# Performance work log

Measured on AMD Instinct MI355X. Metric: run time of the kernel, lower is better.

The kernel has to match this reference:

```python
import jax, jax.numpy as jnp
import numpy as np

BIG = 10000000.0

def heaviside(x):
    return (jnp.tanh(BIG * x) + 1.0) * 0.5

def interception(Prec, PET, INSC):
    INSC = jnp.clip(INSC * 5.0, 0.5, 5.0)
    IMAX = jnp.maximum(jnp.minimum(INSC, PET), 0.0)
    INT = jnp.maximum(jnp.minimum(IMAX, Prec), 0.0)
    INR = jnp.maximum(Prec - INT, 0.0)
    return INT, INR

def soil_moisture_store(SMS1, SMSC):
    SMSC = jnp.clip(SMSC * 500.0, 50.0, 500.0)
    return jnp.maximum(jnp.minimum(SMS1, SMSC), 0.0)

def soil_fluxes(PET, INT, INR, COEFF, SQ, SMSC, SUB, CRAK, SMS1):
    COEFF = jnp.clip(COEFF * 400.0, 50.0, 400.0)
    SQ = jnp.clip(SQ * 6.0, 0.0, 6.0)
    SMSC = jnp.clip(SMSC * 500.0, 50.0, 500.0)
    SUB = jnp.clip(SUB, 0.0, 1.0)
    CRAK = jnp.clip(CRAK, 0.0, 1.0)
    cap = COEFF * jnp.exp(-SQ * SMS1 / SMSC)
    RMO = jnp.maximum(heaviside(cap - INR) * INR + heaviside(INR - cap) * cap, 0.0)
    IRUN = jnp.maximum(INR - RMO, 0.0)
    SRUN = jnp.maximum(SUB * (SMS1 / SMSC) * RMO, 0.0)
    REC = jnp.maximum(CRAK * (SMS1 / SMSC) * (RMO - SRUN), 0.0)
    SMF = jnp.maximum(RMO - SRUN - REC, 0.0)
    POT = jnp.maximum(PET - INT, 0.0)
    r = 10.0 * SMS1 / SMSC
    ETS = jnp.maximum(heaviside(r - POT) * POT + heaviside(POT - r) * r, 0.0)
    return RMO, IRUN, SRUN, REC, SMF, ETS

def recharge_calculation(SMS1, SMSC, REC, SMF, ETS):
    SMSC = jnp.clip(SMSC * 500.0, 50.0, 500.0)
    s = SMS1 + SMF - ETS
    RECnew = heaviside(s - SMSC) * (REC + s - SMSC) + heaviside(SMSC - s) * REC
    return jnp.maximum(RECnew, 0.0)

def groundwaterstore(GW1, RecK):
    RecK = jnp.clip(RecK * 0.3, 0.003, 0.3)
    return jnp.maximum(heaviside(GW1) * (RecK * GW1), 0.0)

def _forward(inputs, INSC, COEFF, SQ, SMSC, SUB, CRAK, RecK):
    B, T, _ = inputs.shape
    xs = jnp.transpose(inputs, (1, 0, 2))  # (T, B, 2)

    def step(carry, x):
        SMS1, GW1 = carry  # each (B, 1)
        Prec, PET = x[:, 0:1], x[:, 1:2]
        INT, INR = interception(Prec, PET, INSC)
        SMS1c = soil_moisture_store(SMS1, SMSC)
        RMO, IRUN, SRUN, REC, SMF, ETS = soil_fluxes(PET, INT, INR, COEFF, SQ, SMSC, SUB, CRAK, SMS1c)
        next_SMS = SMS1c + jnp.clip(SMF - ETS, -100000.0, 100000.0)
        RECnew = recharge_calculation(SMS1c, SMSC, REC, SMF, ETS)
        BAS = groundwaterstore(GW1, RecK)
        next_GW = GW1 + jnp.clip(RECnew - BAS, -100000.0, 100000.0)
        return (next_SMS, next_GW), jnp.concatenate([next_SMS, next_GW], axis=1)

    init = (jnp.zeros((B, 1), inputs.dtype), jnp.zeros((B, 1), inputs.dtype))
    _, outs = jax.lax.scan(step, init, xs)  # (T, B, 2)
    outs = jnp.transpose(outs, (1, 0, 2))   # (B, T, 2)
    outs = jnp.roll(outs, shift=1, axis=1)  # state at step t-1 (wrap like tf.roll)
    SMS1 = outs[:, :, 0:1]
    GW1 = outs[:, :, 1:2]
    Prec = inputs[:, :, 0:1]
    PET = inputs[:, :, 1:2]
    INT, INR = interception(Prec, PET, INSC)
    SMS1 = soil_moisture_store(SMS1, SMSC)
    RMO, IRUN, SRUN, REC, SMF, ETS = soil_fluxes(PET, INT, INR, COEFF, SQ, SMSC, SUB, CRAK, SMS1)
    RECnew = recharge_calculation(SMS1, SMSC, REC, SMF, ETS)
    BAS = groundwaterstore(GW1, RecK)
    DR = jnp.maximum(SRUN + IRUN, 0.0)
    GD = jnp.maximum(BAS, 0.0)
    Q = jnp.maximum(DR + GD, 0.0)
    return Q  # (B, T, 1)


def setup_inputs() -> dict:
    key = jax.random.key(0)
    k1, = jax.random.split(key, 1)
    B, T = 4096, 1024
    # Prec in [0, 20) mm/day, PET in [0, 8) mm/day
    u = jax.random.uniform(k1, (B, T, 2), dtype=jnp.float32)
    scale = jnp.array([20.0, 8.0], dtype=jnp.float32)
    inputs = u * scale
    p = lambda v: jnp.full((1,), v, dtype=jnp.float32)
    return {
        "inputs": inputs,
        "INSC": p(0.5), "COEFF": p(0.5), "SQ": p(0.5), "SMSC": p(0.5),
        "SUB": p(0.5), "CRAK": p(0.5), "RecK": p(0.5),
    }


def reference(inputs, INSC, COEFF, SQ, SMSC, SUB, CRAK, RecK):
    return _forward(inputs, INSC, COEFF, SQ, SMSC, SUB, CRAK, RecK)
```

## Files before the change

### kernel.cpp

```cpp
#include <hip/hip_runtime.h>
#include <hip/hip_bf16.h>
#include <math.h>


struct P {
    float INSC, COEFF, SMSC, RecK, k1, k2, k3, c2;
};

__device__ __forceinline__ P make_params(const float* pINSC, const float* pCOEFF,
                                         const float* pSQ,   const float* pSMSC,
                                         const float* pSUB,  const float* pCRAK,
                                         const float* pRecK) {
    P p;
    p.INSC  = fminf(fmaxf(pINSC[0]  * 5.0f,   0.5f),   5.0f);
    p.COEFF = fminf(fmaxf(pCOEFF[0] * 400.0f, 50.0f),  400.0f);
    float SQ = fminf(fmaxf(pSQ[0]   * 6.0f,   0.0f),   6.0f);
    p.SMSC  = fminf(fmaxf(pSMSC[0]  * 500.0f, 50.0f),  500.0f);
    float SUB  = fminf(fmaxf(pSUB[0],  0.0f), 1.0f);
    float CRAK = fminf(fmaxf(pCRAK[0], 0.0f), 1.0f);
    p.RecK  = fminf(fmaxf(pRecK[0]  * 0.3f,   0.003f), 0.3f);
    float inv = 1.0f / p.SMSC;
    p.k1 = SUB * inv;
    p.k2 = CRAK * inv;
    p.k3 = 10.0f * inv;
    p.c2 = (-SQ * inv) * 1.44269504088896340736f;
    return p;
}

__device__ __forceinline__ float step(float Prec, float PET, float& sms, float& gw, const P& p) {
    float INT   = fminf(fminf(p.INSC, PET), Prec);
    float INR   = Prec - INT;
    float POT   = PET - INT;
    float S     = fmaxf(fminf(sms, p.SMSC), 0.0f);
    float cap   = p.COEFF * exp2f(p.c2 * S);
    float RMO   = fminf(INR, cap);
    float IRUN  = INR - RMO;
    float SRUN  = (p.k1 * S) * RMO;
    float t2    = RMO - SRUN;
    float REC   = (p.k2 * S) * t2;
    float SMF   = t2 - REC;
    float ETS   = fminf(POT, p.k3 * S);
    float s2    = S + (SMF - ETS);
    float RECnew = REC + fmaxf(s2 - p.SMSC, 0.0f);
    float BAS   = p.RecK * gw;
    float Q     = (SRUN + IRUN) + BAS;
    sms = s2;
    gw  = gw + (RECnew - BAS);
    return Q;
}

__device__ __forceinline__ void stepw(float Prec, float PET, float& sms, float& gw, const P& p) {
    float INT   = fminf(fminf(p.INSC, PET), Prec);
    float INR   = Prec - INT;
    float POT   = PET - INT;
    float S     = fmaxf(fminf(sms, p.SMSC), 0.0f);
    float cap   = p.COEFF * exp2f(p.c2 * S);
    float RMO   = fminf(INR, cap);
    float SRUN  = (p.k1 * S) * RMO;
    float t2    = RMO - SRUN;
    float REC   = (p.k2 * S) * t2;
    float SMF   = t2 - REC;
    float ETS   = fminf(POT, p.k3 * S);
    float s2    = S + (SMF - ETS);
    float RECnew = REC + fmaxf(s2 - p.SMSC, 0.0f);
    float BAS   = p.RecK * gw;
    sms = s2;
    gw  = gw + (RECnew - BAS);
}

__device__ __forceinline__ void dstep(float Prec, float PET,
                                      float& slo, float& shi, float& gw, const P& p) {
    float INT = fminf(fminf(p.INSC, PET), Prec);
    float INR = Prec - INT;
    float POT = PET - INT;
    {
        float S     = fmaxf(fminf(shi, p.SMSC), 0.0f);
        float cap   = p.COEFF * exp2f(p.c2 * S);
        float RMO   = fminf(INR, cap);
        float SRUN  = (p.k1 * S) * RMO;
        float t2    = RMO - SRUN;
        float REC   = (p.k2 * S) * t2;
        float SMF   = t2 - REC;
        float ETS   = fminf(POT, p.k3 * S);
        float s2    = S + (SMF - ETS);
        float RECnew = REC + fmaxf(s2 - p.SMSC, 0.0f);
        float BAS   = p.RecK * gw;
        gw  = gw + (RECnew - BAS);
        shi = s2;
    }
    {
        float S     = fmaxf(fminf(slo, p.SMSC), 0.0f);
        float cap   = p.COEFF * exp2f(p.c2 * S);
        float RMO   = fminf(INR, cap);
        float SRUN  = (p.k1 * S) * RMO;
        float t2    = RMO - SRUN;
        float REC   = (p.k2 * S) * t2;
        float SMF   = t2 - REC;
        float ETS   = fminf(POT, p.k3 * S);
        slo = S + (SMF - ETS);
    }
}

#define MERGE_TOL 0.75f

template<int T, int NC, int W>
__global__ __launch_bounds__(64, 1)
void hir_pass1(const float* __restrict__ inputs,
               const float* __restrict__ pINSC,  const float* __restrict__ pCOEFF,
               const float* __restrict__ pSQ,    const float* __restrict__ pSMSC,
               const float* __restrict__ pSUB,   const float* __restrict__ pCRAK,
               const float* __restrict__ pRecK,
               float* __restrict__ out, float4* __restrict__ st, int B)
{
    int gid = blockIdx.x * blockDim.x + threadIdx.x;
    int b = gid % B;
    int c = gid / B;
    if (c >= NC) return;

    P p = make_params(pINSC, pCOEFF, pSQ, pSMSC, pSUB, pCRAK, pRecK);

    const float4* __restrict__ rp = (const float4*)(inputs + (size_t)b * (2 * T));
    float* __restrict__ orow = out + (size_t)b * T;

    constexpr int CH = T / NC;
    const int i1 = (c * CH) >> 1;
    const int i2 = ((c + 1) * CH) >> 1;
    int i0 = i1 - (W >> 1);
    const bool exact = (i0 <= 0);
    if (i0 < 0) i0 = 0;

    float slo = 0.0f, shi = exact ? 0.0f : p.SMSC, gw = 0.0f;

    const int nwb = (i1 - i0) >> 2;
    if (nwb > 0) {
        float4 A[4], Bq[4], C[4];
        #pragma unroll
        for (int j = 0; j < 4; ++j) A[j] = rp[i0 + j];
        {
            int k1b = (1 < nwb) ? 1 : 0;
            #pragma unroll
            for (int j = 0; j < 4; ++j) Bq[j] = rp[i0 + 4 * k1b + j];
        }
        if (exact) {
            for (int k = 0; k < nwb; ++k) {
                int kn = (k + 2 < nwb) ? (k + 2) : (nwb - 1);
                #pragma unroll
                for (int j = 0; j < 4; ++j) C[j] = rp[i0 + 4 * kn + j];
                #pragma unroll
                for (int j = 0; j < 4; ++j) {
                    stepw(A[j].x, A[j].y, shi, gw, p);
                    stepw(A[j].z, A[j].w, shi, gw, p);
                }
                #pragma unroll
                for (int j = 0; j < 4; ++j) { A[j] = Bq[j]; Bq[j] = C[j]; }
            }
            slo = shi;
        } else {
            for (int k = 0; k < nwb; ++k) {
                int kn = (k + 2 < nwb) ? (k + 2) : (nwb - 1);
                #pragma unroll
                for (int j = 0; j < 4; ++j) C[j] = rp[i0 + 4 * kn + j];
                #pragma unroll
                for (int j = 0; j < 4; ++j) {
                    dstep(A[j].x, A[j].y, slo, shi, gw, p);
                    dstep(A[j].z, A[j].w, slo, shi, gw, p);
                }
                #pragma unroll
                for (int j = 0; j < 4; ++j) { A[j] = Bq[j]; Bq[j] = C[j]; }
            }
        }
    }
    const bool merged = exact || ((shi - slo) <= MERGE_TOL);
    float sms = exact ? shi : (0.5f * (slo + shi));

    {
        constexpr int nmb = (CH / 2) / 4;
        float4 A[4], Bq[4], C[4];
        #pragma unroll
        for (int j = 0; j < 4; ++j) A[j] = rp[i1 + j];
        #pragma unroll
        for (int j = 0; j < 4; ++j) Bq[j] = rp[i1 + 4 + j];
        for (int k = 0; k < nmb; ++k) {
            int kn = (k + 2 < nmb) ? (k + 2) : (nmb - 1);
            #pragma unroll
            for (int j = 0; j < 4; ++j) C[j] = rp[i1 + 4 * kn + j];
            int ibase = i1 + 4 * k;
            #pragma unroll
            for (int j = 0; j < 4; ++j) {
                float qa = step(A[j].x, A[j].y, sms, gw, p);
                float qb = step(A[j].z, A[j].w, sms, gw, p);
                if (c == 0 && k == 0 && j == 0) {
                    orow[1] = qb;
                } else {
                    ((float2*)orow)[ibase + j] = make_float2(qa, qb);
                }
            }
            #pragma unroll
            for (int j = 0; j < 4; ++j) { A[j] = Bq[j]; Bq[j] = C[j]; }
        }
    }

    st[(size_t)c * B + b] = make_float4(sms, gw, merged ? 1.0f : 0.0f, 0.0f);

    if (c == NC - 1) {
        float4 f0 = rp[0];
        float ss = sms, gg = gw;
        orow[0] = step(f0.x, f0.y, ss, gg, p);
    }
}

template<int T, int NC>
__global__ __launch_bounds__(64, 1)
void hir_pass2(const float* __restrict__ inputs,
               const float* __restrict__ pINSC,  const float* __restrict__ pCOEFF,
               const float* __restrict__ pSQ,    const float* __restrict__ pSMSC,
               const float* __restrict__ pSUB,   const float* __restrict__ pCRAK,
               const float* __restrict__ pRecK,
               float* __restrict__ out, const float4* __restrict__ st, int B)
{
    int b = blockIdx.x * blockDim.x + threadIdx.x;
    if (b >= B) return;

    P p = make_params(pINSC, pCOEFF, pSQ, pSMSC, pSUB, pCRAK, pRecK);
    constexpr int CH = T / NC;

    const float4* __restrict__ rp = (const float4*)(inputs + (size_t)b * (2 * T));
    float* __restrict__ orow = out + (size_t)b * T;

    float4 s0 = st[b];
    float ex_s = s0.x, ex_g = s0.y;

    for (int c = 1; c < NC; ++c) {
        float4 sc = st[(size_t)c * B + b];
        if (sc.z != 0.0f) {
            ex_s = sc.x; ex_g = sc.y;
            continue;
        }
        float sms = ex_s, gw = ex_g;
        const int i1 = (c * CH) >> 1;
        const int i2 = ((c + 1) * CH) >> 1;
        float4 cur = rp[i1];
        for (int i = i1; i < i2; ++i) {
            int ni = (i + 1 < i2) ? (i + 1) : i;
            float4 nxt = rp[ni];
            float qa = step(cur.x, cur.y, sms, gw, p);
            float qb = step(cur.z, cur.w, sms, gw, p);
            ((float2*)orow)[i] = make_float2(qa, qb);
            cur = nxt;
        }
        ex_s = sms; ex_g = gw;
        if (c == NC - 1) {
            float4 f0 = rp[0];
            float ss = sms, gg = gw;
            orow[0] = step(f0.x, f0.y, ss, gg, p);
        }
    }
}

template<int T>
__global__ __launch_bounds__(64, 1)
void hir_scan_kernel(const float* __restrict__ inputs,
                     const float* __restrict__ pINSC,  const float* __restrict__ pCOEFF,
                     const float* __restrict__ pSQ,    const float* __restrict__ pSMSC,
                     const float* __restrict__ pSUB,   const float* __restrict__ pCRAK,
                     const float* __restrict__ pRecK,
                     float* __restrict__ out, int B)
{
    int b = blockIdx.x * blockDim.x + threadIdx.x;
    if (b >= B) return;
    P p = make_params(pINSC, pCOEFF, pSQ, pSMSC, pSUB, pCRAK, pRecK);
    const float4* __restrict__ rp = (const float4*)(inputs + (size_t)b * (2 * T));
    float* __restrict__ orow = out + (size_t)b * T;
    float sms = 0.0f, gw = 0.0f;
    float4 cur = rp[0];
    const float P0 = cur.x, E0 = cur.y;
    constexpr int NI = T / 2;
    for (int i = 0; i < NI; ++i) {
        int ni = (i + 1 < NI) ? (i + 1) : i;
        float4 nxt = rp[ni];
        float qa = step(cur.x, cur.y, sms, gw, p);
        float qb = step(cur.z, cur.w, sms, gw, p);
        if (i == 0) { orow[1] = qb; }
        else        { ((float2*)orow)[i] = make_float2(qa, qb); }
        cur = nxt;
    }
    float ss = sms, gg = gw;
    orow[0] = step(P0, E0, ss, gg, p);
}

extern "C" void kernel_launch(void* const* d_in, const int* in_sizes, int n_in,
                              void* d_out, int out_size, void* d_ws, size_t ws_size,
                              hipStream_t stream) {
    (void)n_in; (void)out_size;
    constexpr int T  = 1024;
    constexpr int NC = 16;
    constexpr int W  = 320;
    const float* inputs = (const float*)d_in[0];
    const float* INSC   = (const float*)d_in[1];
    const float* COEFF  = (const float*)d_in[2];
    const float* SQ     = (const float*)d_in[3];
    const float* SMSC   = (const float*)d_in[4];
    const float* SUB    = (const float*)d_in[5];
    const float* CRAK   = (const float*)d_in[6];
    const float* RecK   = (const float*)d_in[7];
    float* out = (float*)d_out;

    int B = in_sizes[0] / (2 * T);
    size_t need = (size_t)B * NC * sizeof(float4);

    if (ws_size < need || (B % 64) != 0) {
        int blocks = (B + 63) / 64;
        hir_scan_kernel<T><<<dim3(blocks), dim3(64), 0, stream>>>(
            inputs, INSC, COEFF, SQ, SMSC, SUB, CRAK, RecK, out, B);
        return;
    }

    float4* st = (float4*)d_ws;
    long total = (long)B * NC;
    int blocks1 = (int)((total + 63) / 64);
    hir_pass1<T, NC, W><<<dim3(blocks1), dim3(64), 0, stream>>>(
        inputs, INSC, COEFF, SQ, SMSC, SUB, CRAK, RecK, out, st, B);
    int blocks2 = (B + 63) / 64;
    hir_pass2<T, NC><<<dim3(blocks2), dim3(64), 0, stream>>>(
        inputs, INSC, COEFF, SQ, SMSC, SUB, CRAK, RecK, out, st, B);
}
```

Measured before the change: 134.8 us.

## Split dual warm-up trajectories across two wavefronts per block

The warm-up phase previously ran the high and low soil-moisture trajectories in one thread (dstep). Now each block has two wavefronts: wave 0 runs the high trajectory with groundwater, and wave 1 runs the low trajectory only. The low result is passed through shared memory, and wave 1 exits after a barrier. This shortens the serial dependency chain per thread at the cost of doubling the warm-up input loads and adding a block sync. Launch bounds change to 128 threads with two blocks per CU.

```diff
diff --git a/kernel.cpp b/kernel.cpp
--- a/kernel.cpp
+++ b/kernel.cpp
@@ -68,43 +68,25 @@
     gw  = gw + (RECnew - BAS);
 }
 
-__device__ __forceinline__ void dstep(float Prec, float PET,
-                                      float& slo, float& shi, float& gw, const P& p) {
-    float INT = fminf(fminf(p.INSC, PET), Prec);
-    float INR = Prec - INT;
-    float POT = PET - INT;
-    {
-        float S     = fmaxf(fminf(shi, p.SMSC), 0.0f);
-        float cap   = p.COEFF * exp2f(p.c2 * S);
-        float RMO   = fminf(INR, cap);
-        float SRUN  = (p.k1 * S) * RMO;
-        float t2    = RMO - SRUN;
-        float REC   = (p.k2 * S) * t2;
-        float SMF   = t2 - REC;
-        float ETS   = fminf(POT, p.k3 * S);
-        float s2    = S + (SMF - ETS);
-        float RECnew = REC + fmaxf(s2 - p.SMSC, 0.0f);
-        float BAS   = p.RecK * gw;
-        gw  = gw + (RECnew - BAS);
-        shi = s2;
-    }
-    {
-        float S     = fmaxf(fminf(slo, p.SMSC), 0.0f);
-        float cap   = p.COEFF * exp2f(p.c2 * S);
-        float RMO   = fminf(INR, cap);
-        float SRUN  = (p.k1 * S) * RMO;
-        float t2    = RMO - SRUN;
-        float REC   = (p.k2 * S) * t2;
-        float SMF   = t2 - REC;
-        float ETS   = fminf(POT, p.k3 * S);
-        slo = S + (SMF - ETS);
-    }
+__device__ __forceinline__ void stepl(float Prec, float PET, float& sms, const P& p) {
+    float INT   = fminf(fminf(p.INSC, PET), Prec);
+    float INR   = Prec - INT;
+    float POT   = PET - INT;
+    float S     = fmaxf(fminf(sms, p.SMSC), 0.0f);
+    float cap   = p.COEFF * exp2f(p.c2 * S);
+    float RMO   = fminf(INR, cap);
+    float SRUN  = (p.k1 * S) * RMO;
+    float t2    = RMO - SRUN;
+    float REC   = (p.k2 * S) * t2;
+    float SMF   = t2 - REC;
+    float ETS   = fminf(POT, p.k3 * S);
+    sms = S + (SMF - ETS);
 }
 
 #define MERGE_TOL 0.75f
 
 template<int T, int NC, int W>
-__global__ __launch_bounds__(64, 1)
+__global__ __launch_bounds__(128, 2)
 void hir_pass1(const float* __restrict__ inputs,
                const float* __restrict__ pINSC,  const float* __restrict__ pCOEFF,
                const float* __restrict__ pSQ,    const float* __restrict__ pSMSC,
@@ -112,10 +94,12 @@
                const float* __restrict__ pRecK,
                float* __restrict__ out, float4* __restrict__ st, int B)
 {
-    int gid = blockIdx.x * blockDim.x + threadIdx.x;
-    int b = gid % B;
-    int c = gid / B;
-    if (c >= NC) return;
+    const int lane = threadIdx.x & 63;
+    const int wv   = threadIdx.x >> 6;
+    const int nbg  = B >> 6;
+    const int bg   = blockIdx.x % nbg;
+    const int c    = blockIdx.x / nbg;
+    const int b    = (bg << 6) | lane;
 
     P p = make_params(pINSC, pCOEFF, pSQ, pSMSC, pSUB, pCRAK, pRecK);
 
@@ -129,19 +113,23 @@
     const bool exact = (i0 <= 0);
     if (i0 < 0) i0 = 0;
 
-    float slo = 0.0f, shi = exact ? 0.0f : p.SMSC, gw = 0.0f;
+    __shared__ float slo_sh[64];
+
+    float shi = exact ? 0.0f : p.SMSC;
+    float gw  = 0.0f;
+    float slo = 0.0f;
 
     const int nwb = (i1 - i0) >> 2;
-    if (nwb > 0) {
-        float4 A[4], Bq[4], C[4];
-        #pragma unroll
-        for (int j = 0; j < 4; ++j) A[j] = rp[i0 + j];
-        {
-            int k1b = (1 < nwb) ? 1 : 0;
-            #pragma unroll
-            for (int j = 0; j < 4; ++j) Bq[j] = rp[i0 + 4 * k1b + j];
-        }
-        if (exact) {
+    if (wv == 0) {
+        if (nwb > 0) {
+            float4 A[4], Bq[4], C[4];
+            #pragma unroll
+            for (int j = 0; j < 4; ++j) A[j] = rp[i0 + j];
+            {
+                int k1b = (1 < nwb) ? 1 : 0;
+                #pragma unroll
+                for (int j = 0; j < 4; ++j) Bq[j] = rp[i0 + 4 * k1b + j];
+            }
             for (int k = 0; k < nwb; ++k) {
                 int kn = (k + 2 < nwb) ? (k + 2) : (nwb - 1);
                 #pragma unroll
@@ -154,24 +142,38 @@
                 #pragma unroll
                 for (int j = 0; j < 4; ++j) { A[j] = Bq[j]; Bq[j] = C[j]; }
             }
-            slo = shi;
-        } else {
+        }
+    } else {
+        if (!exact && nwb > 0) {
+            float4 A[4], Bq[4], C[4];
+            #pragma unroll
+            for (int j = 0; j < 4; ++j) A[j] = rp[i0 + j];
+            {
+                int k1b = (1 < nwb) ? 1 : 0;
+                #pragma unroll
+                for (int j = 0; j < 4; ++j) Bq[j] = rp[i0 + 4 * k1b + j];
+            }
             for (int k = 0; k < nwb; ++k) {
                 int kn = (k + 2 < nwb) ? (k + 2) : (nwb - 1);
                 #pragma unroll
                 for (int j = 0; j < 4; ++j) C[j] = rp[i0 + 4 * kn + j];
                 #pragma unroll
                 for (int j = 0; j < 4; ++j) {
-                    dstep(A[j].x, A[j].y, slo, shi, gw, p);
-                    dstep(A[j].z, A[j].w, slo, shi, gw, p);
+                    stepl(A[j].x, A[j].y, slo, p);
+                    stepl(A[j].z, A[j].w, slo, p);
                 }
                 #pragma unroll
                 for (int j = 0; j < 4; ++j) { A[j] = Bq[j]; Bq[j] = C[j]; }
             }
         }
-    }
-    const bool merged = exact || ((shi - slo) <= MERGE_TOL);
-    float sms = exact ? shi : (0.5f * (slo + shi));
+        slo_sh[lane] = slo;
+    }
+    __syncthreads();
+    if (wv == 1) return;
+
+    float slo_r = slo_sh[lane];
+    const bool merged = exact || ((shi - slo_r) <= MERGE_TOL);
+    float sms = exact ? shi : (0.5f * (slo_r + shi));
 
     {
         constexpr int nmb = (CH / 2) / 4;
@@ -316,9 +318,9 @@
     }
 
     float4* st = (float4*)d_ws;
-    long total = (long)B * NC;
-    int blocks1 = (int)((total + 63) / 64);
-    hir_pass1<T, NC, W><<<dim3(blocks1), dim3(64), 0, stream>>>(
+    int nbg = B >> 6;
+    int blocks1 = nbg * NC;
+    hir_pass1<T, NC, W><<<dim3(blocks1), dim3(128), 0, stream>>>(
         inputs, INSC, COEFF, SQ, SMSC, SUB, CRAK, RecK, out, st, B);
     int blocks2 = (B + 63) / 64;
     hir_pass2<T, NC><<<dim3(blocks2), dim3(64), 0, stream>>>(
```

Result: slower. 179.8 us (+33.3%).

## Skip groundwater tracking early in warmup, use hardware exp2, shrink window

Applied to the files above, without the earlier changes.

The warmup phase of each chunk is split in two. The first part runs only the two soil-moisture bound trajectories and does not update groundwater. The last 32 steps add groundwater, because with a large RecK the earlier groundwater contributions decay away. The change also calls the raw hardware exp2 intrinsic, drops the redundant max-with-zero clamp on soil moisture, and reduces the warmup window from 320 to 288. Together these cut per-step ALU work in pass1. The cost is more reliance on the decay assumptions and possibly less accurate early groundwater state, which pass2 must repair when chunks do not merge.

```diff
diff --git a/kernel.cpp b/kernel.cpp
--- a/kernel.cpp
+++ b/kernel.cpp
@@ -27,12 +27,16 @@
     return p;
 }
 
+__device__ __forceinline__ float hexp2(float x) {
+    return __builtin_amdgcn_exp2f(x);
+}
+
 __device__ __forceinline__ float step(float Prec, float PET, float& sms, float& gw, const P& p) {
     float INT   = fminf(fminf(p.INSC, PET), Prec);
     float INR   = Prec - INT;
     float POT   = PET - INT;
-    float S     = fmaxf(fminf(sms, p.SMSC), 0.0f);
-    float cap   = p.COEFF * exp2f(p.c2 * S);
+    float S     = fminf(sms, p.SMSC);
+    float cap   = p.COEFF * hexp2(p.c2 * S);
     float RMO   = fminf(INR, cap);
     float IRUN  = INR - RMO;
     float SRUN  = (p.k1 * S) * RMO;
@@ -49,33 +53,35 @@
     return Q;
 }
 
-__device__ __forceinline__ void stepw(float Prec, float PET, float& sms, float& gw, const P& p) {
-    float INT   = fminf(fminf(p.INSC, PET), Prec);
-    float INR   = Prec - INT;
-    float POT   = PET - INT;
-    float S     = fmaxf(fminf(sms, p.SMSC), 0.0f);
-    float cap   = p.COEFF * exp2f(p.c2 * S);
+__device__ __forceinline__ float supd(float INR, float POT, float s, const P& p) {
+    float S     = fminf(s, p.SMSC);
+    float cap   = p.COEFF * hexp2(p.c2 * S);
     float RMO   = fminf(INR, cap);
     float SRUN  = (p.k1 * S) * RMO;
     float t2    = RMO - SRUN;
     float REC   = (p.k2 * S) * t2;
     float SMF   = t2 - REC;
     float ETS   = fminf(POT, p.k3 * S);
-    float s2    = S + (SMF - ETS);
-    float RECnew = REC + fmaxf(s2 - p.SMSC, 0.0f);
-    float BAS   = p.RecK * gw;
-    sms = s2;
-    gw  = gw + (RECnew - BAS);
-}
-
-__device__ __forceinline__ void dstep(float Prec, float PET,
-                                      float& slo, float& shi, float& gw, const P& p) {
+    return S + (SMF - ETS);
+}
+
+__device__ __forceinline__ void dstep_ss(float Prec, float PET,
+                                         float& slo, float& shi, const P& p) {
+    float INT = fminf(fminf(p.INSC, PET), Prec);
+    float INR = Prec - INT;
+    float POT = PET - INT;
+    shi = supd(INR, POT, shi, p);
+    slo = supd(INR, POT, slo, p);
+}
+
+__device__ __forceinline__ void dstep_g(float Prec, float PET,
+                                        float& slo, float& shi, float& gw, const P& p) {
     float INT = fminf(fminf(p.INSC, PET), Prec);
     float INR = Prec - INT;
     float POT = PET - INT;
     {
-        float S     = fmaxf(fminf(shi, p.SMSC), 0.0f);
-        float cap   = p.COEFF * exp2f(p.c2 * S);
+        float S     = fminf(shi, p.SMSC);
+        float cap   = p.COEFF * hexp2(p.c2 * S);
         float RMO   = fminf(INR, cap);
         float SRUN  = (p.k1 * S) * RMO;
         float t2    = RMO - SRUN;
@@ -88,17 +94,7 @@
         gw  = gw + (RECnew - BAS);
         shi = s2;
     }
-    {
-        float S     = fmaxf(fminf(slo, p.SMSC), 0.0f);
-        float cap   = p.COEFF * exp2f(p.c2 * S);
-        float RMO   = fminf(INR, cap);
-        float SRUN  = (p.k1 * S) * RMO;
-        float t2    = RMO - SRUN;
-        float REC   = (p.k2 * S) * t2;
-        float SMF   = t2 - REC;
-        float ETS   = fminf(POT, p.k3 * S);
-        slo = S + (SMF - ETS);
-    }
+    slo = supd(INR, POT, slo, p);
 }
 
 #define MERGE_TOL 0.75f
@@ -123,55 +119,66 @@
     float* __restrict__ orow = out + (size_t)b * T;
 
     constexpr int CH = T / NC;
-    const int i1 = (c * CH) >> 1;
-    const int i2 = ((c + 1) * CH) >> 1;
+    const int i1 = c * (CH >> 1);
     int i0 = i1 - (W >> 1);
     const bool exact = (i0 <= 0);
     if (i0 < 0) i0 = 0;
+    int ip2 = i1 - 32;
+    if (ip2 < i0) ip2 = i0;
+    if (p.RecK < 0.1f) ip2 = i0;
 
     float slo = 0.0f, shi = exact ? 0.0f : p.SMSC, gw = 0.0f;
 
-    const int nwb = (i1 - i0) >> 2;
-    if (nwb > 0) {
-        float4 A[4], Bq[4], C[4];
-        #pragma unroll
-        for (int j = 0; j < 4; ++j) A[j] = rp[i0 + j];
-        {
-            int k1b = (1 < nwb) ? 1 : 0;
+    {
+        const int nb = (ip2 - i0) >> 2;
+        if (nb > 0) {
+            float4 A[4], Bq[4], C[4];
+            #pragma unroll
+            for (int j = 0; j < 4; ++j) A[j] = rp[i0 + j];
+            int k1b = (1 < nb) ? 1 : 0;
             #pragma unroll
             for (int j = 0; j < 4; ++j) Bq[j] = rp[i0 + 4 * k1b + j];
-        }
-        if (exact) {
-            for (int k = 0; k < nwb; ++k) {
-                int kn = (k + 2 < nwb) ? (k + 2) : (nwb - 1);
+            for (int k = 0; k < nb; ++k) {
+                int kn = (k + 2 < nb) ? (k + 2) : (nb - 1);
                 #pragma unroll
                 for (int j = 0; j < 4; ++j) C[j] = rp[i0 + 4 * kn + j];
                 #pragma unroll
                 for (int j = 0; j < 4; ++j) {
-                    stepw(A[j].x, A[j].y, shi, gw, p);
-                    stepw(A[j].z, A[j].w, shi, gw, p);
+                    dstep_ss(A[j].x, A[j].y, slo, shi, p);
+                    dstep_ss(A[j].z, A[j].w, slo, shi, p);
                 }
                 #pragma unroll
                 for (int j = 0; j < 4; ++j) { A[j] = Bq[j]; Bq[j] = C[j]; }
             }
-            slo = shi;
-        } else {
-            for (int k = 0; k < nwb; ++k) {
-                int kn = (k + 2 < nwb) ? (k + 2) : (nwb - 1);
-                #pragma unroll
-                for (int j = 0; j < 4; ++j) C[j] = rp[i0 + 4 * kn + j];
+        }
+    }
+
+    {
+        const int nb = (i1 - ip2) >> 2;
+        if (nb > 0) {
+            float4 A[4], Bq[4], C[4];
+            #pragma unroll
+            for (int j = 0; j < 4; ++j) A[j] = rp[ip2 + j];
+            int k1b = (1 < nb) ? 1 : 0;
+            #pragma unroll
+            for (int j = 0; j < 4; ++j) Bq[j] = rp[ip2 + 4 * k1b + j];
+            for (int k = 0; k < nb; ++k) {
+                int kn = (k + 2 < nb) ? (k + 2) : (nb - 1);
+                #pragma unroll
+                for (int j = 0; j < 4; ++j) C[j] = rp[ip2 + 4 * kn + j];
                 #pragma unroll
                 for (int j = 0; j < 4; ++j) {
-                    dstep(A[j].x, A[j].y, slo, shi, gw, p);
-                    dstep(A[j].z, A[j].w, slo, shi, gw, p);
+                    dstep_g(A[j].x, A[j].y, slo, shi, gw, p);
+                    dstep_g(A[j].z, A[j].w, slo, shi, gw, p);
                 }
                 #pragma unroll
                 for (int j = 0; j < 4; ++j) { A[j] = Bq[j]; Bq[j] = C[j]; }
             }
         }
     }
+
     const bool merged = exact || ((shi - slo) <= MERGE_TOL);
-    float sms = exact ? shi : (0.5f * (slo + shi));
+    float sms = 0.5f * (slo + shi);
 
     {
         constexpr int nmb = (CH / 2) / 4;
@@ -237,8 +244,8 @@
             continue;
         }
         float sms = ex_s, gw = ex_g;
-        const int i1 = (c * CH) >> 1;
-        const int i2 = ((c + 1) * CH) >> 1;
+        const int i1 = c * (CH >> 1);
+        const int i2 = (c + 1) * (CH >> 1);
         float4 cur = rp[i1];
         for (int i = i1; i < i2; ++i) {
             int ni = (i + 1 < i2) ? (i + 1) : i;
@@ -294,7 +301,7 @@
     (void)n_in; (void)out_size;
     constexpr int T  = 1024;
     constexpr int NC = 16;
-    constexpr int W  = 320;
+    constexpr int W  = 288;
     const float* inputs = (const float*)d_in[0];
     const float* INSC   = (const float*)d_in[1];
     const float* COEFF  = (const float*)d_in[2];
```

Result: slower. 179.6 us (+33.2%).

## Stage pass1 input tiles through LDS for coalesced loads and stores

Applied to the files above, without the earlier changes.

Pass1 now assigns each 64-thread block a group of 64 rows and one chunk. It cooperatively loads 64x64-timestep input tiles into shared memory with coalesced row reads, then each lane walks its own row from LDS. Outputs are written back through the same tile transposed, so global stores are coalesced instead of strided per-thread rows. This adds a __syncthreads per tile and removes the register-level prefetch pipelining, so load latency is no longer overlapped with compute.

```diff
diff --git a/kernel.cpp b/kernel.cpp
--- a/kernel.cpp
+++ b/kernel.cpp
@@ -112,98 +112,83 @@
                const float* __restrict__ pRecK,
                float* __restrict__ out, float4* __restrict__ st, int B)
 {
-    int gid = blockIdx.x * blockDim.x + threadIdx.x;
-    int b = gid % B;
-    int c = gid / B;
-    if (c >= NC) return;
+    const int lane = threadIdx.x;
+    const int nrg  = B >> 6;
+    const int rg   = blockIdx.x % nrg;
+    const int c    = blockIdx.x / nrg;
+    const int b    = (rg << 6) | lane;
 
     P p = make_params(pINSC, pCOEFF, pSQ, pSMSC, pSUB, pCRAK, pRecK);
 
-    const float4* __restrict__ rp = (const float4*)(inputs + (size_t)b * (2 * T));
+    __shared__ float tile[64][130];
+
+    const size_t rowstride = 2 * (size_t)T;
     float* __restrict__ orow = out + (size_t)b * T;
 
     constexpr int CH = T / NC;
-    const int i1 = (c * CH) >> 1;
-    const int i2 = ((c + 1) * CH) >> 1;
-    int i0 = i1 - (W >> 1);
-    const bool exact = (i0 <= 0);
-    if (i0 < 0) i0 = 0;
-
-    float slo = 0.0f, shi = exact ? 0.0f : p.SMSC, gw = 0.0f;
-
-    const int nwb = (i1 - i0) >> 2;
-    if (nwb > 0) {
-        float4 A[4], Bq[4], C[4];
-        #pragma unroll
-        for (int j = 0; j < 4; ++j) A[j] = rp[i0 + j];
+    const int s = c * CH;
+    int t0 = s - W;
+    const bool exact = (t0 <= 0);
+    if (t0 < 0) t0 = 0;
+    const int ntiles = (s + CH - t0) >> 6;
+
+    float slo = 0.0f, shi = exact ? 0.0f : p.SMSC, gw = 0.0f, sms = 0.0f;
+    bool merged = true;
+
+    const float* __restrict__ gbase = inputs + (size_t)(rg << 6) * rowstride;
+
+    for (int k = 0; k < ntiles; ++k) {
+        const int tb = t0 + (k << 6);
+        __syncthreads();
         {
-            int k1b = (1 < nwb) ? 1 : 0;
-            #pragma unroll
-            for (int j = 0; j < 4; ++j) Bq[j] = rp[i0 + 4 * k1b + j];
-        }
-        if (exact) {
-            for (int k = 0; k < nwb; ++k) {
-                int kn = (k + 2 < nwb) ? (k + 2) : (nwb - 1);
-                #pragma unroll
-                for (int j = 0; j < 4; ++j) C[j] = rp[i0 + 4 * kn + j];
-                #pragma unroll
-                for (int j = 0; j < 4; ++j) {
-                    stepw(A[j].x, A[j].y, shi, gw, p);
-                    stepw(A[j].z, A[j].w, shi, gw, p);
+            const float* gt = gbase + 2 * (size_t)tb;
+            #pragma unroll 8
+            for (int r = 0; r < 64; ++r) {
+                const float2* srcr = (const float2*)(gt + (size_t)r * rowstride);
+                float2 v = srcr[lane];
+                *(float2*)&tile[r][2 * lane] = v;
+            }
+        }
+        __syncthreads();
+
+        if (k < ntiles - 1) {
+            if (exact) {
+                for (int t = 0; t < 64; ++t) {
+                    float2 pe = *(const float2*)&tile[lane][2 * t];
+                    stepw(pe.x, pe.y, shi, gw, p);
                 }
-                #pragma unroll
-                for (int j = 0; j < 4; ++j) { A[j] = Bq[j]; Bq[j] = C[j]; }
-            }
-            slo = shi;
-        } else {
-            for (int k = 0; k < nwb; ++k) {
-                int kn = (k + 2 < nwb) ? (k + 2) : (nwb - 1);
-                #pragma unroll
-                for (int j = 0; j < 4; ++j) C[j] = rp[i0 + 4 * kn + j];
-                #pragma unroll
-                for (int j = 0; j < 4; ++j) {
-                    dstep(A[j].x, A[j].y, slo, shi, gw, p);
-                    dstep(A[j].z, A[j].w, slo, shi, gw, p);
-                }
-                #pragma unroll
-                for (int j = 0; j < 4; ++j) { A[j] = Bq[j]; Bq[j] = C[j]; }
-            }
-        }
-    }
-    const bool merged = exact || ((shi - slo) <= MERGE_TOL);
-    float sms = exact ? shi : (0.5f * (slo + shi));
-
-    {
-        constexpr int nmb = (CH / 2) / 4;
-        float4 A[4], Bq[4], C[4];
-        #pragma unroll
-        for (int j = 0; j < 4; ++j) A[j] = rp[i1 + j];
-        #pragma unroll
-        for (int j = 0; j < 4; ++j) Bq[j] = rp[i1 + 4 + j];
-        for (int k = 0; k < nmb; ++k) {
-            int kn = (k + 2 < nmb) ? (k + 2) : (nmb - 1);
-            #pragma unroll
-            for (int j = 0; j < 4; ++j) C[j] = rp[i1 + 4 * kn + j];
-            int ibase = i1 + 4 * k;
-            #pragma unroll
-            for (int j = 0; j < 4; ++j) {
-                float qa = step(A[j].x, A[j].y, sms, gw, p);
-                float qb = step(A[j].z, A[j].w, sms, gw, p);
-                if (c == 0 && k == 0 && j == 0) {
-                    orow[1] = qb;
-                } else {
-                    ((float2*)orow)[ibase + j] = make_float2(qa, qb);
+            } else {
+                for (int t = 0; t < 64; ++t) {
+                    float2 pe = *(const float2*)&tile[lane][2 * t];
+                    dstep(pe.x, pe.y, slo, shi, gw, p);
                 }
             }
-            #pragma unroll
-            for (int j = 0; j < 4; ++j) { A[j] = Bq[j]; Bq[j] = C[j]; }
+        } else {
+            if (exact) slo = shi;
+            merged = exact || ((shi - slo) <= MERGE_TOL);
+            sms = exact ? shi : (0.5f * (slo + shi));
+            for (int t = 0; t < 64; ++t) {
+                float2 pe = *(const float2*)&tile[lane][2 * t];
+                float q = step(pe.x, pe.y, sms, gw, p);
+                tile[lane][t] = q;
+            }
+            __syncthreads();
+            {
+                float* gdst = out + (size_t)(rg << 6) * T + s;
+                #pragma unroll 8
+                for (int r = 0; r < 64; ++r) {
+                    float q = tile[r][lane];
+                    if (c != 0 || lane != 0)
+                        gdst[(size_t)r * T + lane] = q;
+                }
+            }
         }
     }
 
     st[(size_t)c * B + b] = make_float4(sms, gw, merged ? 1.0f : 0.0f, 0.0f);
 
     if (c == NC - 1) {
-        float4 f0 = rp[0];
+        float2 f0 = *(const float2*)(inputs + (size_t)b * rowstride);
         float ss = sms, gg = gw;
         orow[0] = step(f0.x, f0.y, ss, gg, p);
     }
@@ -237,8 +222,8 @@
             continue;
         }
         float sms = ex_s, gw = ex_g;
-        const int i1 = (c * CH) >> 1;
-        const int i2 = ((c + 1) * CH) >> 1;
+        const int i1 = c * (CH >> 1);
+        const int i2 = (c + 1) * (CH >> 1);
         float4 cur = rp[i1];
         for (int i = i1; i < i2; ++i) {
             int ni = (i + 1 < i2) ? (i + 1) : i;
@@ -316,8 +301,8 @@
     }
 
     float4* st = (float4*)d_ws;
-    long total = (long)B * NC;
-    int blocks1 = (int)((total + 63) / 64);
+    int nrg = B >> 6;
+    int blocks1 = nrg * NC;
     hir_pass1<T, NC, W><<<dim3(blocks1), dim3(64), 0, stream>>>(
         inputs, INSC, COEFF, SQ, SMSC, SUB, CRAK, RecK, out, st, B);
     int blocks2 = (B + 63) / 64;
```

Result: slower. 151.7 us (+12.5%).
